# Performance work log

Measured on AMD Instinct MI355X. Metric: run time of the kernel, lower is better.

Reference implementation:

```python
import jax, jax.numpy as jnp
import numpy as np

B, S, D = 2, 2048, 1024
H, DH = 16, 64
FF = 4 * D
EPS = 1e-5
SCALE = 1.0 / np.sqrt(DH)


def setup_inputs() -> dict:
    key = jax.random.key(0)
    ks = jax.random.split(key, 8)
    std = 0.02
    return {
        "x": jax.random.normal(ks[0], (B, S, D), jnp.float32),
        "ln1_g": jnp.ones((D,), jnp.float32),
        "ln1_b": jnp.zeros((D,), jnp.float32),
        "w_qkv": jax.random.normal(ks[1], (D, 3 * H * DH), jnp.float32) * std,
        "b_qkv": jnp.zeros((3 * H * DH,), jnp.float32),
        "w_ao": jax.random.normal(ks[2], (H * DH, D), jnp.float32) * std,
        "b_ao": jnp.zeros((D,), jnp.float32),
        "ln2_g": jnp.ones((D,), jnp.float32),
        "ln2_b": jnp.zeros((D,), jnp.float32),
        "w_fc": jax.random.normal(ks[3], (D, FF), jnp.float32) * std,
        "b_fc": jnp.zeros((FF,), jnp.float32),
        "w_proj": jax.random.normal(ks[4], (FF, D), jnp.float32) * std,
        "b_proj": jnp.zeros((D,), jnp.float32),
    }


def _layernorm(x, g, b):
    mu = jnp.mean(x, axis=-1, keepdims=True)
    var = jnp.mean(jnp.square(x - mu), axis=-1, keepdims=True)
    return (x - mu) * jax.lax.rsqrt(var + EPS) * g + b


def reference(x, ln1_g, ln1_b, w_qkv, b_qkv, w_ao, b_ao,
              ln2_g, ln2_b, w_fc, b_fc, w_proj, b_proj):
    # pre-LN attention
    h = _layernorm(x, ln1_g, ln1_b)
    qkv = h @ w_qkv + b_qkv                      # [B,S,3*H*DH]
    q, k, v = jnp.split(qkv, 3, axis=-1)
    def heads(t):                                 # [B,S,H*DH] -> [B,H,S,DH]
        return t.reshape(B, S, H, DH).transpose(0, 2, 1, 3)
    q, k, v = heads(q), heads(k), heads(v)
    scores = jnp.einsum("bhsd,bhtd->bhst", q, k) * SCALE  # full [B,H,S,S]
    probs = jax.nn.softmax(scores, axis=-1)
    attn = jnp.einsum("bhst,bhtd->bhsd", probs, v)        # [B,H,S,DH]
    attn = attn.transpose(0, 2, 1, 3).reshape(B, S, H * DH)
    attn = attn @ w_ao + b_ao
    x = x + attn
    # pre-LN MLP (exact erf GELU, matches nn.GELU())
    h = _layernorm(x, ln2_g, ln2_b)
    h = jax.nn.gelu(h @ w_fc + b_fc, approximate=False)
    h = h @ w_proj + b_proj
    return x + h
```

## Files before the change

### kernel.cpp

```cpp
#include <hip/hip_runtime.h>
#include <hip/hip_bf16.h>

using short8 = __attribute__((ext_vector_type(8))) short;
using f32x4  = __attribute__((ext_vector_type(4))) float;

#define DEV __device__ __forceinline__

DEV unsigned short f2b(float f) {
  union { float f; unsigned u; } cv; cv.f = f;
  unsigned r = (cv.u + 0x7fffu + ((cv.u >> 16) & 1u)) >> 16;
  return (unsigned short)r;
}

typedef const __attribute__((address_space(1))) unsigned int* gp1;
typedef __attribute__((address_space(3))) unsigned int* lp3;
DEV void gl16(const void* g, void* l) {
  __builtin_amdgcn_global_load_lds((gp1)g, (lp3)l, 16, 0, 0);
}

__global__ void k_tcvt4(const float* __restrict__ s0, unsigned short* __restrict__ d0,
                        const float* __restrict__ s1, unsigned short* __restrict__ d1,
                        const float* __restrict__ s2, unsigned short* __restrict__ d2,
                        const float* __restrict__ s3, unsigned short* __restrict__ d3) {
  __shared__ float tile[32][33];
  int id = blockIdx.x;
  const float* src; unsigned short* dst; int K, N, nx;
  if (id < 3072)      { src = s0; dst = d0; K = 1024; N = 3072; nx = 96; }
  else if (id < 4096) { id -= 3072; src = s1; dst = d1; K = 1024; N = 1024; nx = 32; }
  else if (id < 8192) { id -= 4096; src = s2; dst = d2; K = 1024; N = 4096; nx = 128; }
  else                { id -= 8192; src = s3; dst = d3; K = 4096; N = 1024; nx = 32; }
  int n0 = (id % nx) * 32, k0 = (id / nx) * 32;
  int tx = threadIdx.x, ty = threadIdx.y;
#pragma unroll
  for (int j = 0; j < 4; ++j)
    tile[ty + j * 8][tx] = src[(size_t)(k0 + ty + j * 8) * N + (n0 + tx)];
  __syncthreads();
#pragma unroll
  for (int j = 0; j < 4; ++j)
    dst[(size_t)(n0 + ty + j * 8) * K + (k0 + tx)] = f2b(tile[tx][ty + j * 8]);
}

__global__ __launch_bounds__(256) void k_ln(const float* __restrict__ x,
                                            const float* __restrict__ g,
                                            const float* __restrict__ b,
                                            unsigned short* __restrict__ y) {
  int row = blockIdx.x, tid = threadIdx.x;
  float4 v = reinterpret_cast<const float4*>(x + (size_t)row * 1024)[tid];
  float s  = v.x + v.y + v.z + v.w;
  float s2 = v.x * v.x + v.y * v.y + v.z * v.z + v.w * v.w;
#pragma unroll
  for (int m = 1; m < 64; m <<= 1) { s += __shfl_xor(s, m); s2 += __shfl_xor(s2, m); }
  __shared__ float ps[8];
  int w = tid >> 6;
  if ((tid & 63) == 0) { ps[w] = s; ps[4 + w] = s2; }
  __syncthreads();
  s  = ps[0] + ps[1] + ps[2] + ps[3];
  s2 = ps[4] + ps[5] + ps[6] + ps[7];
  float mu   = s * (1.0f / 1024.0f);
  float var  = fmaxf(s2 * (1.0f / 1024.0f) - mu * mu, 0.f);
  float rstd = rsqrtf(var + 1e-5f);
  float4 gv = reinterpret_cast<const float4*>(g)[tid];
  float4 bv = reinterpret_cast<const float4*>(b)[tid];
  ushort4 o;
  o.x = f2b((v.x - mu) * rstd * gv.x + bv.x);
  o.y = f2b((v.y - mu) * rstd * gv.y + bv.y);
  o.z = f2b((v.z - mu) * rstd * gv.z + bv.z);
  o.w = f2b((v.w - mu) * rstd * gv.w + bv.w);
  reinterpret_cast<ushort4*>(y + (size_t)row * 1024)[tid] = o;
}

enum { EPI_QKV = 0, EPI_RESID = 1, EPI_GELU = 2 };

template <int EPI>
__global__ __launch_bounds__(512, 2) void k_gemm256(
    const unsigned short* __restrict__ A, const unsigned short* __restrict__ BT,
    const float* __restrict__ bias, int M, int N, int K,
    unsigned short* __restrict__ outb,
    unsigned short* __restrict__ qb, unsigned short* __restrict__ kb,
    unsigned short* __restrict__ vb) {
  __shared__ __align__(16) unsigned short Abuf[2][256][64];
  __shared__ __align__(16) unsigned short Bbuf[2][256][64];
  int nx = gridDim.x, nwg = nx * gridDim.y;
  int w0 = blockIdx.y * nx + blockIdx.x;
  int id = (w0 & 7) * (nwg >> 3) + (w0 >> 3);
  int bx = id % nx, by = id / nx;
  int m0 = by * 256, n0 = bx * 256;
  int tid = threadIdx.x;
  int lane = tid & 63, wid = tid >> 6;
  int wm = wid >> 2, wn = wid & 3;
  int l15 = lane & 15, g = lane >> 4;
  int swl = l15 & 7;
  int lrow = lane >> 3;
  int lchunk = (lane & 7) ^ lrow;
  const unsigned short* Asrc = A  + (size_t)(m0 + wid * 32 + lrow) * K + lchunk * 8;
  const unsigned short* Bsrc = BT + (size_t)(n0 + wid * 32 + lrow) * K + lchunk * 8;
  auto stage = [&](int buf, int k0) {
#pragma unroll
    for (int i = 0; i < 4; ++i)
      gl16(Asrc + k0 + (size_t)i * 8 * K, &Abuf[buf][wid * 32 + i * 8][0]);
#pragma unroll
    for (int i = 0; i < 4; ++i)
      gl16(Bsrc + k0 + (size_t)i * 8 * K, &Bbuf[buf][wid * 32 + i * 8][0]);
  };
  f32x4 acc[8][4] = {};
  int nt = K >> 6;
  stage(0, 0);
  stage(1, 64);
  asm volatile("s_waitcnt vmcnt(8)" ::: "memory");
  __builtin_amdgcn_sched_barrier(0);
  __builtin_amdgcn_s_barrier();
  int cur = 0;
  for (int t = 0; t < nt; ++t) {
    const unsigned short (*As)[64] = Abuf[cur];
    const unsigned short (*Bs)[64] = Bbuf[cur];
    short8 a0[8], b0[4], a1[8], b1[4];
#pragma unroll
    for (int mi = 0; mi < 8; ++mi)
      a0[mi] = *reinterpret_cast<const short8*>(&As[wm * 128 + mi * 16 + l15][(g ^ swl) * 8]);
#pragma unroll
    for (int ni = 0; ni < 4; ++ni)
      b0[ni] = *reinterpret_cast<const short8*>(&Bs[wn * 64 + ni * 16 + l15][(g ^ swl) * 8]);
    __builtin_amdgcn_s_setprio(1);
#pragma unroll
    for (int mi = 0; mi < 8; ++mi)
#pragma unroll
      for (int ni = 0; ni < 4; ++ni)
        acc[mi][ni] = __builtin_amdgcn_mfma_f32_16x16x32_bf16(a0[mi], b0[ni], acc[mi][ni], 0, 0, 0);
    __builtin_amdgcn_s_setprio(0);
#pragma unroll
    for (int mi = 0; mi < 8; ++mi)
      a1[mi] = *reinterpret_cast<const short8*>(&As[wm * 128 + mi * 16 + l15][((4 + g) ^ swl) * 8]);
#pragma unroll
    for (int ni = 0; ni < 4; ++ni)
      b1[ni] = *reinterpret_cast<const short8*>(&Bs[wn * 64 + ni * 16 + l15][((4 + g) ^ swl) * 8]);
    asm volatile("s_waitcnt lgkmcnt(0)" ::: "memory");
    __builtin_amdgcn_sched_barrier(0);
    __builtin_amdgcn_s_barrier();
    __builtin_amdgcn_sched_barrier(0);
    if (t + 2 < nt) stage(cur, (t + 2) << 6);
    __builtin_amdgcn_s_setprio(1);
#pragma unroll
    for (int mi = 0; mi < 8; ++mi)
#pragma unroll
      for (int ni = 0; ni < 4; ++ni)
        acc[mi][ni] = __builtin_amdgcn_mfma_f32_16x16x32_bf16(a1[mi], b1[ni], acc[mi][ni], 0, 0, 0);
    __builtin_amdgcn_s_setprio(0);
    if (t + 2 < nt) {
      asm volatile("s_waitcnt vmcnt(8)" ::: "memory");
    } else if (t + 1 < nt) {
      asm volatile("s_waitcnt vmcnt(0)" ::: "memory");
    }
    __builtin_amdgcn_sched_barrier(0);
    __builtin_amdgcn_s_barrier();
    cur ^= 1;
  }
#pragma unroll
  for (int mi = 0; mi < 8; ++mi) {
#pragma unroll
    for (int ni = 0; ni < 4; ++ni) {
      int row0 = m0 + wm * 128 + mi * 16 + g * 4;
      int col  = n0 + wn * 64 + ni * 16 + l15;
      float bcol = bias[col];
      if (EPI == EPI_QKV) {
        int which = col >> 10;
        int hc = col & 1023;
        int h = hc >> 6, d = hc & 63;
        int bb = row0 >> 11, ss0 = row0 & 2047;
        if (which == 2) {
          ushort4 pk;
          pk.x = f2b(acc[mi][ni][0] + bcol);
          pk.y = f2b(acc[mi][ni][1] + bcol);
          pk.z = f2b(acc[mi][ni][2] + bcol);
          pk.w = f2b(acc[mi][ni][3] + bcol);
          *reinterpret_cast<ushort4*>(&vb[(((size_t)(bb * 16 + h)) * 64 + d) * 2048 + ss0]) = pk;
        } else {
#pragma unroll
          for (int j = 0; j < 4; ++j) {
            float vv = acc[mi][ni][j] + bcol;
            size_t idx = (((size_t)(bb * 16 + h)) * 2048 + ss0 + j) * 64 + d;
            unsigned short bv_ = f2b(which == 0 ? vv * 0.18033688011112042f : vv);
            if (which == 0) qb[idx] = bv_;
            else            kb[idx] = bv_;
          }
        }
      } else {
#pragma unroll
        for (int j = 0; j < 4; ++j) {
          float vv = acc[mi][ni][j] + bcol;
          float ge = 0.5f * vv * (1.0f + erff(vv * 0.70710678118654752f));
          outb[(size_t)(row0 + j) * N + col] = f2b(ge);
        }
      }
    }
  }
}

__global__ __launch_bounds__(512) void k_gemm512(
    const unsigned short* __restrict__ A, const unsigned short* __restrict__ BT,
    const float* __restrict__ bias, int M, int N, int K,
    float* __restrict__ outf, const float* __restrict__ resid) {
  __shared__ __align__(16) unsigned short Abuf[2][64][64];
  __shared__ __align__(16) unsigned short Bbuf[2][128][64];
  int nx = gridDim.x, nwg = nx * gridDim.y;
  int w0 = blockIdx.y * nx + blockIdx.x;
  int id = (w0 & 7) * (nwg >> 3) + (w0 >> 3);
  int bx = id % nx, by = id / nx;
  int m0 = by * 64, n0 = bx * 128;
  int tid = threadIdx.x;
  int lane = tid & 63, wid = tid >> 6;
  int wm = wid >> 2, wn = wid & 3;
  int l15 = lane & 15, g = lane >> 4;
  int swl = l15 & 7;
  int lrow = lane >> 3;
  int lchunk = (lane & 7) ^ lrow;
  const unsigned short* Asrc = A  + (size_t)(m0 + wid * 8 + lrow) * K + lchunk * 8;
  const unsigned short* Bsrc = BT + (size_t)(n0 + wid * 16 + lrow) * K + lchunk * 8;
  auto stage = [&](int buf, int k0) {
    gl16(Asrc + k0, &Abuf[buf][wid * 8][0]);
#pragma unroll
    for (int i = 0; i < 2; ++i)
      gl16(Bsrc + k0 + (size_t)i * 8 * K, &Bbuf[buf][wid * 16 + i * 8][0]);
  };
  f32x4 acc[2][2] = {};
  int nt = K >> 6;
  stage(0, 0);
  stage(1, 64);
  asm volatile("s_waitcnt vmcnt(3)" ::: "memory");
  __builtin_amdgcn_sched_barrier(0);
  __builtin_amdgcn_s_barrier();
  int cur = 0;
  for (int t = 0; t < nt; ++t) {
    const unsigned short (*As)[64] = Abuf[cur];
    const unsigned short (*Bs)[64] = Bbuf[cur];
    short8 a0[2], b0[2], a1[2], b1[2];
#pragma unroll
    for (int mi = 0; mi < 2; ++mi)
      a0[mi] = *reinterpret_cast<const short8*>(&As[wm * 32 + mi * 16 + l15][(g ^ swl) * 8]);
#pragma unroll
    for (int ni = 0; ni < 2; ++ni)
      b0[ni] = *reinterpret_cast<const short8*>(&Bs[wn * 32 + ni * 16 + l15][(g ^ swl) * 8]);
    __builtin_amdgcn_s_setprio(1);
#pragma unroll
    for (int mi = 0; mi < 2; ++mi)
#pragma unroll
      for (int ni = 0; ni < 2; ++ni)
        acc[mi][ni] = __builtin_amdgcn_mfma_f32_16x16x32_bf16(a0[mi], b0[ni], acc[mi][ni], 0, 0, 0);
    __builtin_amdgcn_s_setprio(0);
#pragma unroll
    for (int mi = 0; mi < 2; ++mi)
      a1[mi] = *reinterpret_cast<const short8*>(&As[wm * 32 + mi * 16 + l15][((4 + g) ^ swl) * 8]);
#pragma unroll
    for (int ni = 0; ni < 2; ++ni)
      b1[ni] = *reinterpret_cast<const short8*>(&Bs[wn * 32 + ni * 16 + l15][((4 + g) ^ swl) * 8]);
    asm volatile("s_waitcnt lgkmcnt(0)" ::: "memory");
    __builtin_amdgcn_sched_barrier(0);
    __builtin_amdgcn_s_barrier();
    __builtin_amdgcn_sched_barrier(0);
    if (t + 2 < nt) stage(cur, (t + 2) << 6);
    __builtin_amdgcn_s_setprio(1);
#pragma unroll
    for (int mi = 0; mi < 2; ++mi)
#pragma unroll
      for (int ni = 0; ni < 2; ++ni)
        acc[mi][ni] = __builtin_amdgcn_mfma_f32_16x16x32_bf16(a1[mi], b1[ni], acc[mi][ni], 0, 0, 0);
    __builtin_amdgcn_s_setprio(0);
    if (t + 2 < nt) {
      asm volatile("s_waitcnt vmcnt(3)" ::: "memory");
    } else if (t + 1 < nt) {
      asm volatile("s_waitcnt vmcnt(0)" ::: "memory");
    }
    __builtin_amdgcn_sched_barrier(0);
    __builtin_amdgcn_s_barrier();
    cur ^= 1;
  }
#pragma unroll
  for (int mi = 0; mi < 2; ++mi) {
#pragma unroll
    for (int ni = 0; ni < 2; ++ni) {
      int row0 = m0 + wm * 32 + mi * 16 + g * 4;
      int col  = n0 + wn * 32 + ni * 16 + l15;
      float bcol = bias[col];
#pragma unroll
      for (int j = 0; j < 4; ++j) {
        size_t idx = (size_t)(row0 + j) * N + col;
        outf[idx] = acc[mi][ni][j] + bcol + resid[idx];
      }
    }
  }
}

__global__ __launch_bounds__(512) void k_attn(
    const unsigned short* __restrict__ qb, const unsigned short* __restrict__ kb,
    const unsigned short* __restrict__ vt, unsigned short* __restrict__ attn_out) {
  __shared__ __align__(16) unsigned short Ks[64][64];
  __shared__ __align__(16) unsigned short Vs[64][64];
  __shared__ __align__(16) unsigned short Plds[8][16][72];
  int bh = blockIdx.y;
  int b = bh >> 4, h = bh & 15;
  int tid = threadIdx.x;
  int lane = tid & 63, wid = tid >> 6;
  int l15 = lane & 15, g = lane >> 4;
  int q0 = blockIdx.x * 128 + wid * 16;
  const unsigned short* Qb = qb + (size_t)bh * 2048 * 64;
  const unsigned short* Kb = kb + (size_t)bh * 2048 * 64;
  const unsigned short* Vt = vt + (size_t)bh * 64 * 2048;
  short8 qf0 = *reinterpret_cast<const short8*>(&Qb[(size_t)(q0 + l15) * 64 + g * 8]);
  short8 qf1 = *reinterpret_cast<const short8*>(&Qb[(size_t)(q0 + l15) * 64 + 32 + g * 8]);
  short8 vones;
#pragma unroll
  for (int i = 0; i < 8; ++i) vones[i] = (short)0x3F80;
  float mj = 0.0f;
  f32x4 o[4] = {};
  f32x4 lacc = {};
  int sr  = wid * 8 + (lane >> 3);
  int scn = (lane & 7) ^ (sr & 7);
  int swl = l15 & 7;
  for (int t0 = 0; t0 < 2048; t0 += 64) {
    __syncthreads();
    gl16(Kb + (size_t)(t0 + sr) * 64 + scn * 8, &Ks[wid * 8][0]);
    gl16(Vt + (size_t)sr * 2048 + t0 + scn * 8, &Vs[wid * 8][0]);
    __syncthreads();
    f32x4 scv[4];
#pragma unroll
    for (int kk = 0; kk < 4; ++kk) {
      short8 kf0 = *reinterpret_cast<const short8*>(&Ks[kk * 16 + l15][(g ^ swl) * 8]);
      short8 kf1 = *reinterpret_cast<const short8*>(&Ks[kk * 16 + l15][((4 + g) ^ swl) * 8]);
      f32x4 z = {};
      z = __builtin_amdgcn_mfma_f32_16x16x32_bf16(kf0, qf0, z, 0, 0, 0);
      scv[kk] = __builtin_amdgcn_mfma_f32_16x16x32_bf16(kf1, qf1, z, 0, 0, 0);
    }
    float p[16];
#pragma unroll
    for (int kk = 0; kk < 4; ++kk)
#pragma unroll
      for (int j = 0; j < 4; ++j)
        p[kk * 4 + j] = __builtin_amdgcn_exp2f(scv[kk][j] - mj);
#pragma unroll
    for (int kk = 0; kk < 4; ++kk) {
      unsigned r0, r1;
      asm("v_cvt_pk_bf16_f32 %0, %1, %2" : "=v"(r0) : "v"(p[kk * 4 + 0]), "v"(p[kk * 4 + 1]));
      asm("v_cvt_pk_bf16_f32 %0, %1, %2" : "=v"(r1) : "v"(p[kk * 4 + 2]), "v"(p[kk * 4 + 3]));
      unsigned long long w = (unsigned long long)r0 | ((unsigned long long)r1 << 32);
      *reinterpret_cast<unsigned long long*>(&Plds[wid][l15][kk * 16 + g * 4]) = w;
    }
    float t0m = fmaxf(fmaxf(scv[0][0], scv[0][1]), fmaxf(scv[0][2], scv[0][3]));
    float t1m = fmaxf(fmaxf(scv[1][0], scv[1][1]), fmaxf(scv[1][2], scv[1][3]));
    float t2m = fmaxf(fmaxf(scv[2][0], scv[2][1]), fmaxf(scv[2][2], scv[2][3]));
    float t3m = fmaxf(fmaxf(scv[3][0], scv[3][1]), fmaxf(scv[3][2], scv[3][3]));
    float mx = fmaxf(fmaxf(t0m, t1m), fmaxf(t2m, t3m));
    mx = fmaxf(mx, __shfl_xor(mx, 16));
    mx = fmaxf(mx, __shfl_xor(mx, 32));
    if (!__all(mx <= mj + 8.0f)) {
      float mnew = fmaxf(mj, mx);
      float ef = __builtin_amdgcn_exp2f(mj - mnew);
      int sb = 20 * g;
      float e0 = __shfl(ef, sb + 0), e1 = __shfl(ef, sb + 1);
      float e2 = __shfl(ef, sb + 2), e3 = __shfl(ef, sb + 3);
#pragma unroll
      for (int ct = 0; ct < 4; ++ct) {
        o[ct][0] *= e0; o[ct][1] *= e1; o[ct][2] *= e2; o[ct][3] *= e3;
      }
      lacc[0] *= e0; lacc[1] *= e1; lacc[2] *= e2; lacc[3] *= e3;
#pragma unroll
      for (int kk = 0; kk < 4; ++kk) {
#pragma unroll
        for (int j = 0; j < 4; ++j)
          p[kk * 4 + j] = __builtin_amdgcn_exp2f(scv[kk][j] - mnew);
        unsigned r0, r1;
        asm("v_cvt_pk_bf16_f32 %0, %1, %2" : "=v"(r0) : "v"(p[kk * 4 + 0]), "v"(p[kk * 4 + 1]));
        asm("v_cvt_pk_bf16_f32 %0, %1, %2" : "=v"(r1) : "v"(p[kk * 4 + 2]), "v"(p[kk * 4 + 3]));
        unsigned long long w = (unsigned long long)r0 | ((unsigned long long)r1 << 32);
        *reinterpret_cast<unsigned long long*>(&Plds[wid][l15][kk * 16 + g * 4]) = w;
      }
      mj = mnew;
    }
    short8 pf0 = *reinterpret_cast<const short8*>(&Plds[wid][l15][g * 8]);
    short8 pf1 = *reinterpret_cast<const short8*>(&Plds[wid][l15][32 + g * 8]);
    lacc = __builtin_amdgcn_mfma_f32_16x16x32_bf16(pf0, vones, lacc, 0, 0, 0);
    lacc = __builtin_amdgcn_mfma_f32_16x16x32_bf16(pf1, vones, lacc, 0, 0, 0);
#pragma unroll
    for (int ct = 0; ct < 4; ++ct) {
      short8 vf0 = *reinterpret_cast<const short8*>(&Vs[ct * 16 + l15][(g ^ swl) * 8]);
      short8 vf1 = *reinterpret_cast<const short8*>(&Vs[ct * 16 + l15][((4 + g) ^ swl) * 8]);
      o[ct] = __builtin_amdgcn_mfma_f32_16x16x32_bf16(pf0, vf0, o[ct], 0, 0, 0);
      o[ct] = __builtin_amdgcn_mfma_f32_16x16x32_bf16(pf1, vf1, o[ct], 0, 0, 0);
    }
  }
#pragma unroll
  for (int j = 0; j < 4; ++j) {
    float iv = 1.0f / lacc[j];
    size_t t = (size_t)b * 2048 + (q0 + g * 4 + j);
#pragma unroll
    for (int ct = 0; ct < 4; ++ct)
      attn_out[t * 1024 + h * 64 + ct * 16 + l15] = f2b(o[ct][j] * iv);
  }
}

extern "C" void kernel_launch(void* const* d_in, const int* in_sizes, int n_in,
                              void* d_out, int out_size, void* d_ws, size_t ws_size,
                              hipStream_t stream) {
  (void)in_sizes; (void)n_in; (void)out_size; (void)ws_size;
  const float* x      = (const float*)d_in[0];
  const float* ln1_g  = (const float*)d_in[1];
  const float* ln1_b  = (const float*)d_in[2];
  const float* w_qkv  = (const float*)d_in[3];
  const float* b_qkv  = (const float*)d_in[4];
  const float* w_ao   = (const float*)d_in[5];
  const float* b_ao   = (const float*)d_in[6];
  const float* ln2_g  = (const float*)d_in[7];
  const float* ln2_b  = (const float*)d_in[8];
  const float* w_fc   = (const float*)d_in[9];
  const float* b_fc   = (const float*)d_in[10];
  const float* w_proj = (const float*)d_in[11];
  const float* b_proj = (const float*)d_in[12];
  float* out = (float*)d_out;

  char* ws = (char*)d_ws;
  size_t o = 0;
  auto nxt = [&](size_t bytes) { void* p = ws + o; o += (bytes + 255) & ~(size_t)255; return p; };
  unsigned short* wT_qkv  = (unsigned short*)nxt((size_t)3072 * 1024 * 2);
  unsigned short* wT_ao   = (unsigned short*)nxt((size_t)1024 * 1024 * 2);
  unsigned short* wT_fc   = (unsigned short*)nxt((size_t)4096 * 1024 * 2);
  unsigned short* wT_proj = (unsigned short*)nxt((size_t)1024 * 4096 * 2);
  unsigned short* h_ln    = (unsigned short*)nxt((size_t)4096 * 1024 * 2);
  unsigned short* qbuf    = (unsigned short*)nxt((size_t)4096 * 1024 * 2);
  unsigned short* kbuf    = (unsigned short*)nxt((size_t)4096 * 1024 * 2);
  unsigned short* vtb     = (unsigned short*)nxt((size_t)4096 * 1024 * 2);
  unsigned short* attn_o  = (unsigned short*)nxt((size_t)4096 * 1024 * 2);
  float*          out1    = (float*)nxt((size_t)4096 * 1024 * 4);
  unsigned short* fc_buf  = qbuf;

  dim3 b32(32, 8, 1);
  k_tcvt4<<<12288, b32, 0, stream>>>(w_qkv, wT_qkv, w_ao, wT_ao, w_fc, wT_fc, w_proj, wT_proj);

  k_ln<<<4096, 256, 0, stream>>>(x, ln1_g, ln1_b, h_ln);
  k_gemm256<EPI_QKV><<<dim3(12, 16), 512, 0, stream>>>(h_ln, wT_qkv, b_qkv, 4096, 3072, 1024,
                                                       nullptr, qbuf, kbuf, vtb);
  k_attn<<<dim3(16, 32), 512, 0, stream>>>(qbuf, kbuf, vtb, attn_o);
  k_gemm512<<<dim3(8, 64), 512, 0, stream>>>(attn_o, wT_ao, b_ao, 4096, 1024, 1024,
                                             out1, x);
  k_ln<<<4096, 256, 0, stream>>>(out1, ln2_g, ln2_b, h_ln);
  k_gemm256<EPI_GELU><<<dim3(16, 16), 512, 0, stream>>>(h_ln, wT_fc, b_fc, 4096, 4096, 1024,
                                                        fc_buf, nullptr, nullptr, nullptr);
  k_gemm512<<<dim3(8, 64), 512, 0, stream>>>(fc_buf, wT_proj, b_proj, 4096, 1024, 4096,
                                             out, out1);
}
```

Measured before the change: 228.8 us.

## Fuse LN1 into weight-transpose kernel and stage 128-key tiles in attention

The first LayerNorm is folded into the weight transpose/convert kernel as extra blocks, which removes one kernel launch and lets the two independent jobs run side by side. In attention, each outer iteration now loads 128 keys and values into LDS instead of 64, then processes them in two 64-wide halves. This halves the number of block-wide barriers per head, at the cost of more shared memory per block, which may lower occupancy.

Measured after the change: 225.0 us (median of 2 runs). No clear change (-1.7%).

```diff
diff --git a/kernel.cpp b/kernel.cpp
--- a/kernel.cpp
+++ b/kernel.cpp
@@ -18,19 +18,48 @@
   __builtin_amdgcn_global_load_lds((gp1)g, (lp3)l, 16, 0, 0);
 }
 
-__global__ void k_tcvt4(const float* __restrict__ s0, unsigned short* __restrict__ d0,
-                        const float* __restrict__ s1, unsigned short* __restrict__ d1,
-                        const float* __restrict__ s2, unsigned short* __restrict__ d2,
-                        const float* __restrict__ s3, unsigned short* __restrict__ d3) {
+__global__ void k_pre(const float* __restrict__ s0, unsigned short* __restrict__ d0,
+                      const float* __restrict__ s1, unsigned short* __restrict__ d1,
+                      const float* __restrict__ s2, unsigned short* __restrict__ d2,
+                      const float* __restrict__ s3, unsigned short* __restrict__ d3,
+                      const float* __restrict__ x, const float* __restrict__ g1,
+                      const float* __restrict__ b1, unsigned short* __restrict__ y) {
   __shared__ float tile[32][33];
+  __shared__ float ps[8];
   int id = blockIdx.x;
+  int tx = threadIdx.x, ty = threadIdx.y;
+  if (id >= 12288) {
+    int row = id - 12288;
+    int tid = ty * 32 + tx;
+    float4 v = reinterpret_cast<const float4*>(x + (size_t)row * 1024)[tid];
+    float s  = v.x + v.y + v.z + v.w;
+    float s2 = v.x * v.x + v.y * v.y + v.z * v.z + v.w * v.w;
+#pragma unroll
+    for (int m = 1; m < 64; m <<= 1) { s += __shfl_xor(s, m); s2 += __shfl_xor(s2, m); }
+    int w = tid >> 6;
+    if ((tid & 63) == 0) { ps[w] = s; ps[4 + w] = s2; }
+    __syncthreads();
+    s  = ps[0] + ps[1] + ps[2] + ps[3];
+    s2 = ps[4] + ps[5] + ps[6] + ps[7];
+    float mu   = s * (1.0f / 1024.0f);
+    float var  = fmaxf(s2 * (1.0f / 1024.0f) - mu * mu, 0.f);
+    float rstd = rsqrtf(var + 1e-5f);
+    float4 gv = reinterpret_cast<const float4*>(g1)[tid];
+    float4 bv = reinterpret_cast<const float4*>(b1)[tid];
+    ushort4 o;
+    o.x = f2b((v.x - mu) * rstd * gv.x + bv.x);
+    o.y = f2b((v.y - mu) * rstd * gv.y + bv.y);
+    o.z = f2b((v.z - mu) * rstd * gv.z + bv.z);
+    o.w = f2b((v.w - mu) * rstd * gv.w + bv.w);
+    reinterpret_cast<ushort4*>(y + (size_t)row * 1024)[tid] = o;
+    return;
+  }
   const float* src; unsigned short* dst; int K, N, nx;
   if (id < 3072)      { src = s0; dst = d0; K = 1024; N = 3072; nx = 96; }
   else if (id < 4096) { id -= 3072; src = s1; dst = d1; K = 1024; N = 1024; nx = 32; }
   else if (id < 8192) { id -= 4096; src = s2; dst = d2; K = 1024; N = 4096; nx = 128; }
   else                { id -= 8192; src = s3; dst = d3; K = 4096; N = 1024; nx = 32; }
   int n0 = (id % nx) * 32, k0 = (id / nx) * 32;
-  int tx = threadIdx.x, ty = threadIdx.y;
 #pragma unroll
   for (int j = 0; j < 4; ++j)
     tile[ty + j * 8][tx] = src[(size_t)(k0 + ty + j * 8) * N + (n0 + tx)];
@@ -292,8 +321,8 @@
 __global__ __launch_bounds__(512) void k_attn(
     const unsigned short* __restrict__ qb, const unsigned short* __restrict__ kb,
     const unsigned short* __restrict__ vt, unsigned short* __restrict__ attn_out) {
-  __shared__ __align__(16) unsigned short Ks[64][64];
-  __shared__ __align__(16) unsigned short Vs[64][64];
+  __shared__ __align__(16) unsigned short Ks[128][64];
+  __shared__ __align__(16) unsigned short Vs[2][64][64];
   __shared__ __align__(16) unsigned short Plds[8][16][72];
   int bh = blockIdx.y;
   int b = bh >> 4, h = bh & 15;
@@ -312,78 +341,85 @@
   float mj = 0.0f;
   f32x4 o[4] = {};
   f32x4 lacc = {};
-  int sr  = wid * 8 + (lane >> 3);
-  int scn = (lane & 7) ^ (sr & 7);
+  int kr  = wid * 16 + (lane >> 3);
+  int kcn = (lane & 7) ^ (kr & 7);
+  int vr  = wid * 8 + (lane >> 3);
+  int vcn = (lane & 7) ^ (vr & 7);
   int swl = l15 & 7;
-  for (int t0 = 0; t0 < 2048; t0 += 64) {
+  for (int t0 = 0; t0 < 2048; t0 += 128) {
     __syncthreads();
-    gl16(Kb + (size_t)(t0 + sr) * 64 + scn * 8, &Ks[wid * 8][0]);
-    gl16(Vt + (size_t)sr * 2048 + t0 + scn * 8, &Vs[wid * 8][0]);
+    gl16(Kb + (size_t)(t0 + kr) * 64 + kcn * 8,      &Ks[wid * 16][0]);
+    gl16(Kb + (size_t)(t0 + kr + 8) * 64 + kcn * 8,  &Ks[wid * 16 + 8][0]);
+    gl16(Vt + (size_t)vr * 2048 + t0 + vcn * 8,      &Vs[0][wid * 8][0]);
+    gl16(Vt + (size_t)vr * 2048 + t0 + 64 + vcn * 8, &Vs[1][wid * 8][0]);
     __syncthreads();
-    f32x4 scv[4];
-#pragma unroll
-    for (int kk = 0; kk < 4; ++kk) {
-      short8 kf0 = *reinterpret_cast<const short8*>(&Ks[kk * 16 + l15][(g ^ swl) * 8]);
-      short8 kf1 = *reinterpret_cast<const short8*>(&Ks[kk * 16 + l15][((4 + g) ^ swl) * 8]);
-      f32x4 z = {};
-      z = __builtin_amdgcn_mfma_f32_16x16x32_bf16(kf0, qf0, z, 0, 0, 0);
-      scv[kk] = __builtin_amdgcn_mfma_f32_16x16x32_bf16(kf1, qf1, z, 0, 0, 0);
-    }
-    float p[16];
-#pragma unroll
-    for (int kk = 0; kk < 4; ++kk)
-#pragma unroll
-      for (int j = 0; j < 4; ++j)
-        p[kk * 4 + j] = __builtin_amdgcn_exp2f(scv[kk][j] - mj);
-#pragma unroll
-    for (int kk = 0; kk < 4; ++kk) {
-      unsigned r0, r1;
-      asm("v_cvt_pk_bf16_f32 %0, %1, %2" : "=v"(r0) : "v"(p[kk * 4 + 0]), "v"(p[kk * 4 + 1]));
-      asm("v_cvt_pk_bf16_f32 %0, %1, %2" : "=v"(r1) : "v"(p[kk * 4 + 2]), "v"(p[kk * 4 + 3]));
-      unsigned long long w = (unsigned long long)r0 | ((unsigned long long)r1 << 32);
-      *reinterpret_cast<unsigned long long*>(&Plds[wid][l15][kk * 16 + g * 4]) = w;
-    }
-    float t0m = fmaxf(fmaxf(scv[0][0], scv[0][1]), fmaxf(scv[0][2], scv[0][3]));
-    float t1m = fmaxf(fmaxf(scv[1][0], scv[1][1]), fmaxf(scv[1][2], scv[1][3]));
-    float t2m = fmaxf(fmaxf(scv[2][0], scv[2][1]), fmaxf(scv[2][2], scv[2][3]));
-    float t3m = fmaxf(fmaxf(scv[3][0], scv[3][1]), fmaxf(scv[3][2], scv[3][3]));
-    float mx = fmaxf(fmaxf(t0m, t1m), fmaxf(t2m, t3m));
-    mx = fmaxf(mx, __shfl_xor(mx, 16));
-    mx = fmaxf(mx, __shfl_xor(mx, 32));
-    if (!__all(mx <= mj + 8.0f)) {
-      float mnew = fmaxf(mj, mx);
-      float ef = __builtin_amdgcn_exp2f(mj - mnew);
-      int sb = 20 * g;
-      float e0 = __shfl(ef, sb + 0), e1 = __shfl(ef, sb + 1);
-      float e2 = __shfl(ef, sb + 2), e3 = __shfl(ef, sb + 3);
-#pragma unroll
-      for (int ct = 0; ct < 4; ++ct) {
-        o[ct][0] *= e0; o[ct][1] *= e1; o[ct][2] *= e2; o[ct][3] *= e3;
-      }
-      lacc[0] *= e0; lacc[1] *= e1; lacc[2] *= e2; lacc[3] *= e3;
+#pragma unroll
+    for (int half = 0; half < 2; ++half) {
+      f32x4 scv[4];
 #pragma unroll
       for (int kk = 0; kk < 4; ++kk) {
+        short8 kf0 = *reinterpret_cast<const short8*>(&Ks[half * 64 + kk * 16 + l15][(g ^ swl) * 8]);
+        short8 kf1 = *reinterpret_cast<const short8*>(&Ks[half * 64 + kk * 16 + l15][((4 + g) ^ swl) * 8]);
+        f32x4 z = {};
+        z = __builtin_amdgcn_mfma_f32_16x16x32_bf16(kf0, qf0, z, 0, 0, 0);
+        scv[kk] = __builtin_amdgcn_mfma_f32_16x16x32_bf16(kf1, qf1, z, 0, 0, 0);
+      }
+      float p[16];
+#pragma unroll
+      for (int kk = 0; kk < 4; ++kk)
 #pragma unroll
         for (int j = 0; j < 4; ++j)
-          p[kk * 4 + j] = __builtin_amdgcn_exp2f(scv[kk][j] - mnew);
+          p[kk * 4 + j] = __builtin_amdgcn_exp2f(scv[kk][j] - mj);
+#pragma unroll
+      for (int kk = 0; kk < 4; ++kk) {
         unsigned r0, r1;
         asm("v_cvt_pk_bf16_f32 %0, %1, %2" : "=v"(r0) : "v"(p[kk * 4 + 0]), "v"(p[kk * 4 + 1]));
         asm("v_cvt_pk_bf16_f32 %0, %1, %2" : "=v"(r1) : "v"(p[kk * 4 + 2]), "v"(p[kk * 4 + 3]));
         unsigned long long w = (unsigned long long)r0 | ((unsigned long long)r1 << 32);
         *reinterpret_cast<unsigned long long*>(&Plds[wid][l15][kk * 16 + g * 4]) = w;
       }
-      mj = mnew;
-    }
-    short8 pf0 = *reinterpret_cast<const short8*>(&Plds[wid][l15][g * 8]);
-    short8 pf1 = *reinterpret_cast<const short8*>(&Plds[wid][l15][32 + g * 8]);
-    lacc = __builtin_amdgcn_mfma_f32_16x16x32_bf16(pf0, vones, lacc, 0, 0, 0);
-    lacc = __builtin_amdgcn_mfma_f32_16x16x32_bf16(pf1, vones, lacc, 0, 0, 0);
-#pragma unroll
-    for (int ct = 0; ct < 4; ++ct) {
-      short8 vf0 = *reinterpret_cast<const short8*>(&Vs[ct * 16 + l15][(g ^ swl) * 8]);
-      short8 vf1 = *reinterpret_cast<const short8*>(&Vs[ct * 16 + l15][((4 + g) ^ swl) * 8]);
-      o[ct] = __builtin_amdgcn_mfma_f32_16x16x32_bf16(pf0, vf0, o[ct], 0, 0, 0);
-      o[ct] = __builtin_amdgcn_mfma_f32_16x16x32_bf16(pf1, vf1, o[ct], 0, 0, 0);
+      float t0m = fmaxf(fmaxf(scv[0][0], scv[0][1]), fmaxf(scv[0][2], scv[0][3]));
+      float t1m = fmaxf(fmaxf(scv[1][0], scv[1][1]), fmaxf(scv[1][2], scv[1][3]));
+      float t2m = fmaxf(fmaxf(scv[2][0], scv[2][1]), fmaxf(scv[2][2], scv[2][3]));
+      float t3m = fmaxf(fmaxf(scv[3][0], scv[3][1]), fmaxf(scv[3][2], scv[3][3]));
+      float mx = fmaxf(fmaxf(t0m, t1m), fmaxf(t2m, t3m));
+      mx = fmaxf(mx, __shfl_xor(mx, 16));
+      mx = fmaxf(mx, __shfl_xor(mx, 32));
+      if (!__all(mx <= mj + 8.0f)) {
+        float mnew = fmaxf(mj, mx);
+        float ef = __builtin_amdgcn_exp2f(mj - mnew);
+        int sb = 20 * g;
+        float e0 = __shfl(ef, sb + 0), e1 = __shfl(ef, sb + 1);
+        float e2 = __shfl(ef, sb + 2), e3 = __shfl(ef, sb + 3);
+#pragma unroll
+        for (int ct = 0; ct < 4; ++ct) {
+          o[ct][0] *= e0; o[ct][1] *= e1; o[ct][2] *= e2; o[ct][3] *= e3;
+        }
+        lacc[0] *= e0; lacc[1] *= e1; lacc[2] *= e2; lacc[3] *= e3;
+#pragma unroll
+        for (int kk = 0; kk < 4; ++kk) {
+#pragma unroll
+          for (int j = 0; j < 4; ++j)
+            p[kk * 4 + j] = __builtin_amdgcn_exp2f(scv[kk][j] - mnew);
+          unsigned r0, r1;
+          asm("v_cvt_pk_bf16_f32 %0, %1, %2" : "=v"(r0) : "v"(p[kk * 4 + 0]), "v"(p[kk * 4 + 1]));
+          asm("v_cvt_pk_bf16_f32 %0, %1, %2" : "=v"(r1) : "v"(p[kk * 4 + 2]), "v"(p[kk * 4 + 3]));
+          unsigned long long w = (unsigned long long)r0 | ((unsigned long long)r1 << 32);
+          *reinterpret_cast<unsigned long long*>(&Plds[wid][l15][kk * 16 + g * 4]) = w;
+        }
+        mj = mnew;
+      }
+      short8 pf0 = *reinterpret_cast<const short8*>(&Plds[wid][l15][g * 8]);
+      short8 pf1 = *reinterpret_cast<const short8*>(&Plds[wid][l15][32 + g * 8]);
+      lacc = __builtin_amdgcn_mfma_f32_16x16x32_bf16(pf0, vones, lacc, 0, 0, 0);
+      lacc = __builtin_amdgcn_mfma_f32_16x16x32_bf16(pf1, vones, lacc, 0, 0, 0);
+#pragma unroll
+      for (int ct = 0; ct < 4; ++ct) {
+        short8 vf0 = *reinterpret_cast<const short8*>(&Vs[half][ct * 16 + l15][(g ^ swl) * 8]);
+        short8 vf1 = *reinterpret_cast<const short8*>(&Vs[half][ct * 16 + l15][((4 + g) ^ swl) * 8]);
+        o[ct] = __builtin_amdgcn_mfma_f32_16x16x32_bf16(pf0, vf0, o[ct], 0, 0, 0);
+        o[ct] = __builtin_amdgcn_mfma_f32_16x16x32_bf16(pf1, vf1, o[ct], 0, 0, 0);
+      }
     }
   }
 #pragma unroll
@@ -431,9 +467,8 @@
   unsigned short* fc_buf  = qbuf;
 
   dim3 b32(32, 8, 1);
-  k_tcvt4<<<12288, b32, 0, stream>>>(w_qkv, wT_qkv, w_ao, wT_ao, w_fc, wT_fc, w_proj, wT_proj);
-
-  k_ln<<<4096, 256, 0, stream>>>(x, ln1_g, ln1_b, h_ln);
+  k_pre<<<16384, b32, 0, stream>>>(w_qkv, wT_qkv, w_ao, wT_ao, w_fc, wT_fc, w_proj, wT_proj,
+                                   x, ln1_g, ln1_b, h_ln);
   k_gemm256<EPI_QKV><<<dim3(12, 16), 512, 0, stream>>>(h_ln, wT_qkv, b_qkv, 4096, 3072, 1024,
                                                        nullptr, qbuf, kbuf, vtb);
   k_attn<<<dim3(16, 32), 512, 0, stream>>>(qbuf, kbuf, vtb, attn_o);
```
